# Kernel optimization log

Hardware: AMD Instinct MI355X
Metric: run time of the kernel (lower is better)

Reference implementation:

```python
import jax, jax.numpy as jnp
import numpy as np

HEADS = 3
NEG_SLOPE = 0.2


def setup_inputs() -> dict:
    key = jax.random.key(0)
    ks = jax.random.split(key, 16)
    B, node_num, his, in_dim = 2, 5000, 12, 2
    N = B * node_num
    E = 160000
    hidden = 32
    C = hidden * his  # 384, per-head out channels of GATConv
    gat_in = in_dim * his  # 24
    s = 0.05
    return {
        "x": jax.random.normal(ks[0], (B, node_num, his, in_dim), jnp.float32),
        "edge_index": jax.random.randint(ks[1], (2, E), 0, N, jnp.int64),
        "lin_w": jax.random.normal(ks[2], (HEADS * C, gat_in), jnp.float32) * s,
        "att_src": jax.random.normal(ks[3], (HEADS, C), jnp.float32) * s,
        "att_dst": jax.random.normal(ks[4], (HEADS, C), jnp.float32) * s,
        "gat_bias": jax.random.normal(ks[5], (C,), jnp.float32) * s,
        "w_ih": jax.random.normal(ks[6], (3 * hidden, hidden), jnp.float32) * s,
        "w_hh": jax.random.normal(ks[7], (3 * hidden, hidden), jnp.float32) * s,
        "b_ih": jax.random.normal(ks[8], (3 * hidden,), jnp.float32) * s,
        "b_hh": jax.random.normal(ks[9], (3 * hidden,), jnp.float32) * s,
        "p1_w": jax.random.normal(ks[10], (1, hidden), jnp.float32) * s,
        "p1_b": jax.random.normal(ks[11], (1,), jnp.float32) * s,
        "p2_w": jax.random.normal(ks[12], (his, his), jnp.float32) * s,
        "p2_b": jax.random.normal(ks[13], (his,), jnp.float32) * s,
    }


def _gat_conv(xf, src, dst, N, lin_w, att_src, att_dst, gat_bias):
    # xf: [N, gat_in]; returns [N, C] (mean over heads, concat=False)
    heads, C = att_src.shape
    h = (xf @ lin_w.T).reshape(N, heads, C)           # [N,heads,C]
    a_src = jnp.einsum('nhc,hc->nh', h, att_src)      # [N,heads]
    a_dst = jnp.einsum('nhc,hc->nh', h, att_dst)
    alpha = jax.nn.leaky_relu(a_src[src] + a_dst[dst], NEG_SLOPE)  # [E,heads]
    # edge softmax over incoming edges of each dst node (stable)
    amax = jax.ops.segment_max(alpha, dst, num_segments=N)
    ea = jnp.exp(alpha - amax[dst])
    denom = jax.ops.segment_sum(ea, dst, num_segments=N)
    w = ea / denom[dst]                               # [E,heads]
    msg = h[src] * w[:, :, None]                      # [E,heads,C] -- dominant traffic
    out = jax.ops.segment_sum(msg, dst, num_segments=N)
    return out.mean(axis=1) + gat_bias                # [N,C]


def _gru(seq, w_ih, w_hh, b_ih, b_hh):
    # seq: [N, T, H] -> outputs [N, T, H], PyTorch GRU gate order (r,z,n)
    N, T, H = seq.shape
    def step(hprev, xt):
        gi = xt @ w_ih.T + b_ih
        gh = hprev @ w_hh.T + b_hh
        ir, iz, inn = jnp.split(gi, 3, axis=-1)
        hr, hz, hn = jnp.split(gh, 3, axis=-1)
        r = jax.nn.sigmoid(ir + hr)
        z = jax.nn.sigmoid(iz + hz)
        n = jnp.tanh(inn + r * hn)
        hnew = (1.0 - z) * n + z * hprev
        return hnew, hnew
    h0 = jnp.zeros((N, H), seq.dtype)
    _, hs = jax.lax.scan(step, h0, seq.transpose(1, 0, 2))
    return hs.transpose(1, 0, 2)


def reference(x, edge_index, lin_w, att_src, att_dst, gat_bias,
              w_ih, w_hh, b_ih, b_hh, p1_w, p1_b, p2_w, p2_b):
    B, node_num, his, in_dim = x.shape
    N = B * node_num
    xf = x.reshape(N, his * in_dim)
    # GATConv adds self-loops (add_self_loops=True default in PyG)
    loops = jnp.arange(N)
    src = jnp.concatenate([edge_index[0], loops])
    dst = jnp.concatenate([edge_index[1], loops])
    gat_out = _gat_conv(xf, src, dst, N, lin_w, att_src, att_dst, gat_bias)  # [N, hidden*his]
    hidden = w_hh.shape[1]
    gru_in = gat_out.reshape(N, his, hidden)
    gru_out = _gru(gru_in, w_ih, w_hh, b_ih, b_hh)    # [N, his, hidden]
    o = (gru_out @ p1_w.T + p1_b).squeeze(-1)         # [N, his]
    o = o @ p2_w.T + p2_b                              # [N, pred_num]
    return o.reshape(B, node_num, -1)
```

## Files before the change

### kernel.cpp

```cpp
#include <hip/hip_runtime.h>
#include <math.h>

#define HEADS 3
#define C_OUT 384
#define GAT_IN 24
#define HID 32
#define TSTEPS 12
#define NEG_SLOPE 0.2f
#define CAPW 64
#define SLOTS 96

typedef __attribute__((ext_vector_type(8))) short bf16x8;
typedef __attribute__((ext_vector_type(4))) float f32x4;

__device__ __forceinline__ float sigm(float x) {
  return 1.f / (1.f + __expf(-x));
}
__device__ __forceinline__ float tanh_fast(float x) {
  return 2.f / (1.f + __expf(-2.f * x)) - 1.f;
}
__device__ __forceinline__ unsigned short f2bf(float x) {
  unsigned int u = __float_as_uint(x);
  unsigned int r = u + 0x7fffu + ((u >> 16) & 1u);
  return (unsigned short)(r >> 16);
}
__device__ __forceinline__ float bf2f(unsigned short u) {
  return __uint_as_float((unsigned int)u << 16);
}
__device__ __forceinline__ float lrelu(float x) {
  return x >= 0.f ? x : NEG_SLOPE * x;
}

__global__ __launch_bounds__(96) void k_const(const float* __restrict__ lin_w,
                                              const float* __restrict__ gat_bias,
                                              const float* __restrict__ wih,
                                              const float* __restrict__ bih,
                                              const float* __restrict__ att_src,
                                              const float* __restrict__ att_dst,
                                              unsigned short* __restrict__ WWt,
                                              float* __restrict__ biasb,
                                              float* __restrict__ vbuf,
                                              int* __restrict__ cnt, int N) {
  int b = blockIdx.x;
  if (b < 876) {
    int t = b / 73, k = b % 73;
    int g = threadIdx.x;
    __shared__ float s_w[32];
    if (g < 32) {
      if (k < 72) {
        int h = k / 24, j = k % 24;
        s_w[g] = lin_w[(size_t)(h * C_OUT + t * 32 + g) * GAT_IN + j] * (1.f / 3.f);
      } else {
        s_w[g] = gat_bias[t * 32 + g];
      }
    }
    __syncthreads();
    const float* wrow = wih + (size_t)g * 32;
    float acc = 0.f;
#pragma unroll
    for (int c = 0; c < 32; ++c) acc += s_w[c] * wrow[c];
    if (k < 72) {
      WWt[((size_t)t * 96 + g) * 96 + k] = f2bf(acc);
      if (k < 24) WWt[((size_t)t * 96 + g) * 96 + 72 + k] = 0;
    } else {
      biasb[t * 96 + g] = acc + bih[g];
    }
  } else if (b < 948) {
    int bb = b - 876;
    int h = bb / 24, j = bb % 24;
    int lane = threadIdx.x;
    if (lane >= 64) return;
    float as = 0.f, ad = 0.f;
    for (int c = lane; c < C_OUT; c += 64) {
      float wv = lin_w[(size_t)(h * C_OUT + c) * GAT_IN + j];
      as += att_src[h * C_OUT + c] * wv;
      ad += att_dst[h * C_OUT + c] * wv;
    }
#pragma unroll
    for (int off = 32; off >= 1; off >>= 1) {
      as += __shfl_xor(as, off, 64);
      ad += __shfl_xor(ad, off, 64);
    }
    if (lane == 0) {
      vbuf[h * 24 + j] = as;
      vbuf[72 + h * 24 + j] = ad;
    }
  } else {
    int i = (b - 948) * 96 + threadIdx.x;
    if (i < N) cnt[i] = 0;
  }
}

__global__ void k_place(const int* __restrict__ esrc,
                        const int* __restrict__ edst, int* __restrict__ cnt,
                        int* __restrict__ slist, int E, int ET) {
  int e = blockIdx.x * blockDim.x + threadIdx.x;
  if (e >= ET) return;
  int d, s;
  if (e < E) { d = edst[e]; s = esrc[e]; }
  else { d = e - E; s = e - E; }
  int pos = atomicAdd(&cnt[d], 1);
  if (pos < SLOTS) slist[(size_t)d * SLOTS + pos] = s;
}

__global__ __launch_bounds__(256) void k_aggx(
    const float* __restrict__ xf, const float* __restrict__ vbuf,
    const int* __restrict__ slist, const int* __restrict__ cnt,
    unsigned short* __restrict__ Yb, int N) {
  __shared__ float s_v[144];
  __shared__ float s_w[4][CAPW][3];
  __shared__ unsigned short s_xb[4][CAPW][26];
  int tid = threadIdx.x, lane = tid & 63, wv = tid >> 6;
  if (tid < 144) s_v[tid] = vbuf[tid];
  __syncthreads();
  int n = blockIdx.x * 4 + wv;
  if (n >= N) return;

  int deg = min(cnt[n], SLOTS);

  float xl = (lane < 24) ? xf[(size_t)n * 24 + lane] : 0.f;
  float ad0, ad1, ad2;
  {
    float p0 = (lane < 24) ? xl * s_v[72 + lane] : 0.f;
    float p1 = (lane < 24) ? xl * s_v[96 + lane] : 0.f;
    float p2 = (lane < 24) ? xl * s_v[120 + lane] : 0.f;
#pragma unroll
    for (int off = 32; off >= 1; off >>= 1) {
      p0 += __shfl_xor(p0, off, 64);
      p1 += __shfl_xor(p1, off, 64);
      p2 += __shfl_xor(p2, off, 64);
    }
    ad0 = p0; ad1 = p1; ad2 = p2;
  }

  float t0 = 0.f, t1 = 0.f, t2 = 0.f;
  for (int i = lane; i < deg; i += 64) {
    int s = slist[(size_t)n * SLOTS + i];
    const float4* xr = (const float4*)(xf + (size_t)s * 24);
    float xs[24];
#pragma unroll
    for (int q = 0; q < 6; ++q) {
      float4 v = xr[q];
      xs[4 * q] = v.x; xs[4 * q + 1] = v.y;
      xs[4 * q + 2] = v.z; xs[4 * q + 3] = v.w;
    }
    float as0 = 0.f, as1 = 0.f, as2 = 0.f;
#pragma unroll
    for (int j = 0; j < 24; ++j) {
      float v = xs[j];
      as0 += v * s_v[j];
      as1 += v * s_v[24 + j];
      as2 += v * s_v[48 + j];
    }
    float e0 = __expf(lrelu(as0 + ad0));
    float e1 = __expf(lrelu(as1 + ad1));
    float e2 = __expf(lrelu(as2 + ad2));
    if (i < CAPW) {
      s_w[wv][i][0] = e0; s_w[wv][i][1] = e1; s_w[wv][i][2] = e2;
#pragma unroll
      for (int j = 0; j < 24; ++j) s_xb[wv][i][j] = f2bf(xs[j]);
    }
    t0 += e0; t1 += e1; t2 += e2;
  }
#pragma unroll
  for (int off = 32; off >= 1; off >>= 1) {
    t0 += __shfl_xor(t0, off, 64);
    t1 += __shfl_xor(t1, off, 64);
    t2 += __shfl_xor(t2, off, 64);
  }
  float inv0 = 1.f / t0, inv1 = 1.f / t1, inv2 = 1.f / t2;

  int eg = lane >> 5;
  int c = lane & 31;
  float acc0 = 0.f, acc1 = 0.f, acc2 = 0.f;
  if (deg <= CAPW) {
    int cc = (c < 24) ? c : 0;
    float cmask = (c < 24) ? 1.f : 0.f;
#pragma unroll 2
    for (int i = eg; i < deg; i += 2) {
      float w0 = s_w[wv][i][0] * inv0;
      float w1 = s_w[wv][i][1] * inv1;
      float w2 = s_w[wv][i][2] * inv2;
      float xv = bf2f(s_xb[wv][i][cc]) * cmask;
      acc0 += w0 * xv; acc1 += w1 * xv; acc2 += w2 * xv;
    }
  } else {
    for (int i = eg; i < deg; i += 2) {
      int s = slist[(size_t)n * SLOTS + i];
      float as0 = 0.f, as1 = 0.f, as2 = 0.f;
      const float* xr = xf + (size_t)s * 24;
#pragma unroll
      for (int j = 0; j < 24; ++j) {
        float v = xr[j];
        as0 += v * s_v[j];
        as1 += v * s_v[24 + j];
        as2 += v * s_v[48 + j];
      }
      float w0 = __expf(lrelu(as0 + ad0)) * inv0;
      float w1 = __expf(lrelu(as1 + ad1)) * inv1;
      float w2 = __expf(lrelu(as2 + ad2)) * inv2;
      float xv = (c < 24) ? xf[(size_t)s * 24 + c] : 0.f;
      acc0 += w0 * xv; acc1 += w1 * xv; acc2 += w2 * xv;
    }
  }
  acc0 += __shfl_xor(acc0, 32, 64);
  acc1 += __shfl_xor(acc1, 32, 64);
  acc2 += __shfl_xor(acc2, 32, 64);
  if (lane < 24) {
    unsigned short* yr = Yb + (size_t)n * 72;
    yr[lane] = f2bf(acc0);
    yr[24 + lane] = f2bf(acc1);
    yr[48 + lane] = f2bf(acc2);
  }
}

__global__ __launch_bounds__(256, 2) void k_gmr(
    const unsigned short* __restrict__ Yb,
    const unsigned short* __restrict__ WWt, const float* __restrict__ biasb,
    const float* __restrict__ whh, const float* __restrict__ bhh,
    const float* __restrict__ p1w, const float* __restrict__ p1b,
    const float* __restrict__ p2w, const float* __restrict__ p2b,
    float* __restrict__ out, int N) {
  __shared__ short A_lds[16][104];
  __shared__ unsigned short gi_lds[12][16][96];
  __shared__ float s_bias[12][96];
  __shared__ float h_buf[4][36];
  __shared__ float s_o[16][12];
  int tid = threadIdx.x;
  int m0 = blockIdx.x * 16;

  const unsigned int* Yu = (const unsigned int*)Yb;
  for (int u = tid; u < 16 * 36; u += 256) {
    int r = u / 36, c2 = u % 36;
    int rc = min(m0 + r, N - 1);
    *(unsigned int*)&A_lds[r][c2 * 2] = Yu[(size_t)rc * 36 + c2];
  }
  if (tid < 256) {
    int r = tid >> 4, c2 = tid & 15;
    *(unsigned int*)&A_lds[r][72 + c2 * 2] = 0;
  }
  for (int u = tid; u < 12 * 96; u += 256) s_bias[u / 96][u % 96] = biasb[u];
  __syncthreads();

  int l = tid & 63, wv = tid >> 6;
  {
    int mrow = l & 15;
    int koff = (l >> 4) * 8;
    bf16x8 a0 = *(const bf16x8*)&A_lds[mrow][koff];
    bf16x8 a1 = *(const bf16x8*)&A_lds[mrow][32 + koff];
    bf16x8 a2 = *(const bf16x8*)&A_lds[mrow][64 + koff];
    int rrow = (l >> 4) * 4;
#pragma unroll
    for (int q = 0; q < 3; ++q) {
      int tt = wv * 3 + q;
#pragma unroll
      for (int nt = 0; nt < 6; ++nt) {
        int col = nt * 16 + (l & 15);
        const unsigned short* bp = WWt + ((size_t)tt * 96 + col) * 96 + koff;
        bf16x8 b0 = *(const bf16x8*)&bp[0];
        bf16x8 b1 = *(const bf16x8*)&bp[32];
        bf16x8 b2 = *(const bf16x8*)&bp[64];
        f32x4 acc = {0.f, 0.f, 0.f, 0.f};
        acc = __builtin_amdgcn_mfma_f32_16x16x32_bf16(a0, b0, acc, 0, 0, 0);
        acc = __builtin_amdgcn_mfma_f32_16x16x32_bf16(a1, b1, acc, 0, 0, 0);
        acc = __builtin_amdgcn_mfma_f32_16x16x32_bf16(a2, b2, acc, 0, 0, 0);
        float bs = s_bias[tt][col];
#pragma unroll
        for (int rg = 0; rg < 4; ++rg)
          gi_lds[tt][rrow + rg][col] = f2bf(acc[rg] + bs);
      }
    }
  }
  __syncthreads();

  int k = l & 31, jh = l >> 5;
  const float4* pr = (const float4*)(whh + (size_t)k * HID + jh * 16);
  const float4* pz = (const float4*)(whh + (size_t)(HID + k) * HID + jh * 16);
  const float4* pn = (const float4*)(whh + (size_t)(2 * HID + k) * HID + jh * 16);
  float4 wr0 = pr[0], wr1 = pr[1], wr2 = pr[2], wr3 = pr[3];
  float4 wz0 = pz[0], wz1 = pz[1], wz2 = pz[2], wz3 = pz[3];
  float4 wn0 = pn[0], wn1 = pn[1], wn2 = pn[2], wn3 = pn[3];
  float bhr = bhh[k], bhz = bhh[HID + k], bhn = bhh[2 * HID + k];
  float p1k = p1w[k];
  float p1b0 = p1b[0];

  for (int i = 0; i < 4; ++i) {
    int nl = wv * 4 + i;
    int node = m0 + nl;
    if (node >= N) break;
    if (jh == 0) h_buf[wv][k] = 0.f;
    float h = 0.f;
    float gr = bf2f(gi_lds[0][nl][k]);
    float gz = bf2f(gi_lds[0][nl][32 + k]);
    float gn = bf2f(gi_lds[0][nl][64 + k]);
    for (int t = 0; t < TSTEPS; ++t) {
      float gr1 = 0.f, gz1 = 0.f, gn1 = 0.f;
      if (t + 1 < TSTEPS) {
        gr1 = bf2f(gi_lds[t + 1][nl][k]);
        gz1 = bf2f(gi_lds[t + 1][nl][32 + k]);
        gn1 = bf2f(gi_lds[t + 1][nl][64 + k]);
      }
      const float* hh = &h_buf[wv][jh * 16];
      float4 h0 = *(const float4*)(hh);
      float4 h1 = *(const float4*)(hh + 4);
      float4 h2 = *(const float4*)(hh + 8);
      float4 h3 = *(const float4*)(hh + 12);
      float ar = wr0.x * h0.x + wr0.y * h0.y + wr0.z * h0.z + wr0.w * h0.w +
                 wr1.x * h1.x + wr1.y * h1.y + wr1.z * h1.z + wr1.w * h1.w +
                 wr2.x * h2.x + wr2.y * h2.y + wr2.z * h2.z + wr2.w * h2.w +
                 wr3.x * h3.x + wr3.y * h3.y + wr3.z * h3.z + wr3.w * h3.w;
      float az = wz0.x * h0.x + wz0.y * h0.y + wz0.z * h0.z + wz0.w * h0.w +
                 wz1.x * h1.x + wz1.y * h1.y + wz1.z * h1.z + wz1.w * h1.w +
                 wz2.x * h2.x + wz2.y * h2.y + wz2.z * h2.z + wz2.w * h2.w +
                 wz3.x * h3.x + wz3.y * h3.y + wz3.z * h3.z + wz3.w * h3.w;
      float an = wn0.x * h0.x + wn0.y * h0.y + wn0.z * h0.z + wn0.w * h0.w +
                 wn1.x * h1.x + wn1.y * h1.y + wn1.z * h1.z + wn1.w * h1.w +
                 wn2.x * h2.x + wn2.y * h2.y + wn2.z * h2.z + wn2.w * h2.w +
                 wn3.x * h3.x + wn3.y * h3.y + wn3.z * h3.z + wn3.w * h3.w;
      ar += __shfl_xor(ar, 32, 64);
      az += __shfl_xor(az, 32, 64);
      an += __shfl_xor(an, 32, 64);
      float r = sigm(gr + ar + bhr);
      float z = sigm(gz + az + bhz);
      float nn = tanh_fast(gn + r * (an + bhn));
      h = (1.f - z) * nn + z * h;
      if (jh == 0) h_buf[wv][k] = h;
      float po = p1k * h;
#pragma unroll
      for (int off = 16; off >= 1; off >>= 1) po += __shfl_xor(po, off, 64);
      if (l == 0) s_o[nl][t] = po + p1b0;
      gr = gr1; gz = gz1; gn = gn1;
    }
    if (l < TSTEPS) {
      float acc = p2b[l];
#pragma unroll
      for (int s2 = 0; s2 < TSTEPS; ++s2)
        acc += p2w[l * TSTEPS + s2] * s_o[nl][s2];
      out[(size_t)node * TSTEPS + l] = acc;
    }
  }
}

extern "C" void kernel_launch(void* const* d_in, const int* in_sizes, int n_in,
                              void* d_out, int out_size, void* d_ws,
                              size_t ws_size, hipStream_t stream) {
  const float* x = (const float*)d_in[0];
  const int* ei = (const int*)d_in[1];
  const float* lin_w = (const float*)d_in[2];
  const float* att_src = (const float*)d_in[3];
  const float* att_dst = (const float*)d_in[4];
  const float* gat_bias = (const float*)d_in[5];
  const float* w_ih = (const float*)d_in[6];
  const float* w_hh = (const float*)d_in[7];
  const float* b_ih = (const float*)d_in[8];
  const float* b_hh = (const float*)d_in[9];
  const float* p1w = (const float*)d_in[10];
  const float* p1b = (const float*)d_in[11];
  const float* p2w = (const float*)d_in[12];
  const float* p2b = (const float*)d_in[13];

  int N = in_sizes[0] / GAT_IN;
  int E = in_sizes[1] / 2;
  int ET = E + N;

  size_t off = 0;
  char* base = (char*)d_ws;
  auto alloc = [&](size_t bytes) {
    void* p = base + off;
    off += (bytes + 255) & ~(size_t)255;
    return p;
  };
  unsigned short* Yb = (unsigned short*)alloc((size_t)N * 72 * 2);
  unsigned short* WWt = (unsigned short*)alloc((size_t)12 * 96 * 96 * 2);
  float* biasb = (float*)alloc((size_t)12 * 96 * 4);
  float* vbuf = (float*)alloc(144 * 4);
  int* cnt = (int*)alloc((size_t)N * 4);
  int* slist = (int*)alloc((size_t)N * SLOTS * 4);
  (void)ws_size; (void)n_in; (void)out_size;

  int zero_blocks = (N + 95) / 96;
  k_const<<<948 + zero_blocks, 96, 0, stream>>>(lin_w, gat_bias, w_ih, b_ih,
                                                att_src, att_dst, WWt, biasb,
                                                vbuf, cnt, N);
  k_place<<<(ET + 255) / 256, 256, 0, stream>>>(ei, ei + E, cnt, slist, E, ET);
  k_aggx<<<(N + 3) / 4, 256, 0, stream>>>(x, vbuf, slist, cnt, Yb, N);
  k_gmr<<<(N + 15) / 16, 256, 0, stream>>>(Yb, WWt, biasb, w_hh, b_hh, p1w,
                                           p1b, p2w, p2b, (float*)d_out, N);
}
```

Baseline: 86.17 us.

## Run GRU recurrence on MFMA per 16-node wavefront, fusing input projection per step

Replaces the 256-thread GRU kernel with a single-wavefront kernel that handles 16 nodes at once. The hidden-state matmul (W_hh·h) now runs on bf16 MFMA across all 16 nodes, with h passed through a small LDS tile each step. The per-timestep input projection is computed inside the time loop instead of being staged into a large LDS buffer. This removes the scalar FMA dot products and the big shared-memory staging, at the cost of rounding W_hh and h to bf16 and adding a barrier every timestep.

```diff
diff --git a/kernel.cpp b/kernel.cpp
--- a/kernel.cpp
+++ b/kernel.cpp
@@ -214,129 +214,111 @@
   }
 }
 
-__global__ __launch_bounds__(256, 2) void k_gmr(
+__global__ __launch_bounds__(64) void k_rec2(
     const unsigned short* __restrict__ Yb,
     const unsigned short* __restrict__ WWt, const float* __restrict__ biasb,
     const float* __restrict__ whh, const float* __restrict__ bhh,
     const float* __restrict__ p1w, const float* __restrict__ p1b,
     const float* __restrict__ p2w, const float* __restrict__ p2b,
     float* __restrict__ out, int N) {
-  __shared__ short A_lds[16][104];
-  __shared__ unsigned short gi_lds[12][16][96];
-  __shared__ float s_bias[12][96];
-  __shared__ float h_buf[4][36];
+  __shared__ unsigned short h16[16][32];
   __shared__ float s_o[16][12];
-  int tid = threadIdx.x;
+  int l = threadIdx.x;
+  int c = l & 15, hi = l >> 4;
   int m0 = blockIdx.x * 16;
 
-  const unsigned int* Yu = (const unsigned int*)Yb;
-  for (int u = tid; u < 16 * 36; u += 256) {
-    int r = u / 36, c2 = u % 36;
-    int rc = min(m0 + r, N - 1);
-    *(unsigned int*)&A_lds[r][c2 * 2] = Yu[(size_t)rc * 36 + c2];
-  }
-  if (tid < 256) {
-    int r = tid >> 4, c2 = tid & 15;
-    *(unsigned int*)&A_lds[r][72 + c2 * 2] = 0;
-  }
-  for (int u = tid; u < 12 * 96; u += 256) s_bias[u / 96][u % 96] = biasb[u];
+  int row = min(m0 + c, N - 1);
+  const unsigned short* yr = Yb + (size_t)row * 72;
+  bf16x8 ya0 = *(const bf16x8*)(yr + hi * 8);
+  bf16x8 ya1 = *(const bf16x8*)(yr + 32 + hi * 8);
+  bf16x8 ya2 = {0, 0, 0, 0, 0, 0, 0, 0};
+  if (hi == 0) ya2 = *(const bf16x8*)(yr + 64);
+
+  bf16x8 wb[6];
+#pragma unroll
+  for (int nt = 0; nt < 6; ++nt) {
+    const float* wp = whh + (size_t)(nt * 16 + c) * 32 + hi * 8;
+#pragma unroll
+    for (int j = 0; j < 8; ++j) wb[nt][j] = (short)f2bf(wp[j]);
+  }
+
+  float bhr0 = bhh[c], bhr1 = bhh[c + 16];
+  float bhz0 = bhh[32 + c], bhz1 = bhh[48 + c];
+  float bhn0 = bhh[64 + c], bhn1 = bhh[80 + c];
+  float p1c0 = p1w[c], p1c1 = p1w[c + 16], p1b0 = p1b[0];
+
+  float hA[4] = {0.f, 0.f, 0.f, 0.f}, hB[4] = {0.f, 0.f, 0.f, 0.f};
+  bf16x8 ha = {0, 0, 0, 0, 0, 0, 0, 0};
+
+  for (int t = 0; t < TSTEPS; ++t) {
+    const unsigned short* Wt = WWt + (size_t)t * 96 * 96;
+    f32x4 g0 = {0,0,0,0}, g1 = {0,0,0,0}, g2 = {0,0,0,0};
+    f32x4 g3 = {0,0,0,0}, g4 = {0,0,0,0}, g5 = {0,0,0,0};
+#pragma unroll
+    for (int q = 0; q < 3; ++q) {
+      bf16x8 aq = (q == 0) ? ya0 : (q == 1) ? ya1 : ya2;
+      int ko = q * 32 + hi * 8;
+      bf16x8 b0 = *(const bf16x8*)(Wt + (size_t)(0 * 16 + c) * 96 + ko);
+      bf16x8 b1 = *(const bf16x8*)(Wt + (size_t)(1 * 16 + c) * 96 + ko);
+      bf16x8 b2 = *(const bf16x8*)(Wt + (size_t)(2 * 16 + c) * 96 + ko);
+      bf16x8 b3 = *(const bf16x8*)(Wt + (size_t)(3 * 16 + c) * 96 + ko);
+      bf16x8 b4 = *(const bf16x8*)(Wt + (size_t)(4 * 16 + c) * 96 + ko);
+      bf16x8 b5 = *(const bf16x8*)(Wt + (size_t)(5 * 16 + c) * 96 + ko);
+      g0 = __builtin_amdgcn_mfma_f32_16x16x32_bf16(aq, b0, g0, 0, 0, 0);
+      g1 = __builtin_amdgcn_mfma_f32_16x16x32_bf16(aq, b1, g1, 0, 0, 0);
+      g2 = __builtin_amdgcn_mfma_f32_16x16x32_bf16(aq, b2, g2, 0, 0, 0);
+      g3 = __builtin_amdgcn_mfma_f32_16x16x32_bf16(aq, b3, g3, 0, 0, 0);
+      g4 = __builtin_amdgcn_mfma_f32_16x16x32_bf16(aq, b4, g4, 0, 0, 0);
+      g5 = __builtin_amdgcn_mfma_f32_16x16x32_bf16(aq, b5, g5, 0, 0, 0);
+    }
+    f32x4 zz = {0,0,0,0};
+    f32x4 h0 = __builtin_amdgcn_mfma_f32_16x16x32_bf16(ha, wb[0], zz, 0, 0, 0);
+    f32x4 h1 = __builtin_amdgcn_mfma_f32_16x16x32_bf16(ha, wb[1], zz, 0, 0, 0);
+    f32x4 h2 = __builtin_amdgcn_mfma_f32_16x16x32_bf16(ha, wb[2], zz, 0, 0, 0);
+    f32x4 h3 = __builtin_amdgcn_mfma_f32_16x16x32_bf16(ha, wb[3], zz, 0, 0, 0);
+    f32x4 h4 = __builtin_amdgcn_mfma_f32_16x16x32_bf16(ha, wb[4], zz, 0, 0, 0);
+    f32x4 h5 = __builtin_amdgcn_mfma_f32_16x16x32_bf16(ha, wb[5], zz, 0, 0, 0);
+    const float* bt = biasb + t * 96;
+    float br0 = bt[c], br1 = bt[16 + c];
+    float bz0 = bt[32 + c], bz1 = bt[48 + c];
+    float bn0 = bt[64 + c], bn1 = bt[80 + c];
+    float po[4];
+#pragma unroll
+    for (int reg = 0; reg < 4; ++reg) {
+      float r0 = sigm(g0[reg] + br0 + h0[reg] + bhr0);
+      float z0 = sigm(g2[reg] + bz0 + h2[reg] + bhz0);
+      float n0 = tanh_fast(g4[reg] + bn0 + r0 * (h4[reg] + bhn0));
+      hA[reg] = (1.f - z0) * n0 + z0 * hA[reg];
+      float r1 = sigm(g1[reg] + br1 + h1[reg] + bhr1);
+      float z1 = sigm(g3[reg] + bz1 + h3[reg] + bhz1);
+      float n1 = tanh_fast(g5[reg] + bn1 + r1 * (h5[reg] + bhn1));
+      hB[reg] = (1.f - z1) * n1 + z1 * hB[reg];
+      h16[hi * 4 + reg][c] = f2bf(hA[reg]);
+      h16[hi * 4 + reg][c + 16] = f2bf(hB[reg]);
+      po[reg] = p1c0 * hA[reg] + p1c1 * hB[reg];
+    }
+#pragma unroll
+    for (int off = 1; off < 16; off <<= 1) {
+#pragma unroll
+      for (int reg = 0; reg < 4; ++reg) po[reg] += __shfl_xor(po[reg], off, 64);
+    }
+    if (c == 0) {
+#pragma unroll
+      for (int reg = 0; reg < 4; ++reg) s_o[hi * 4 + reg][t] = po[reg] + p1b0;
+    }
+    __syncthreads();
+    ha = *(const bf16x8*)&h16[c][hi * 8];
+  }
   __syncthreads();
-
-  int l = tid & 63, wv = tid >> 6;
-  {
-    int mrow = l & 15;
-    int koff = (l >> 4) * 8;
-    bf16x8 a0 = *(const bf16x8*)&A_lds[mrow][koff];
-    bf16x8 a1 = *(const bf16x8*)&A_lds[mrow][32 + koff];
-    bf16x8 a2 = *(const bf16x8*)&A_lds[mrow][64 + koff];
-    int rrow = (l >> 4) * 4;
-#pragma unroll
-    for (int q = 0; q < 3; ++q) {
-      int tt = wv * 3 + q;
-#pragma unroll
-      for (int nt = 0; nt < 6; ++nt) {
-        int col = nt * 16 + (l & 15);
-        const unsigned short* bp = WWt + ((size_t)tt * 96 + col) * 96 + koff;
-        bf16x8 b0 = *(const bf16x8*)&bp[0];
-        bf16x8 b1 = *(const bf16x8*)&bp[32];
-        bf16x8 b2 = *(const bf16x8*)&bp[64];
-        f32x4 acc = {0.f, 0.f, 0.f, 0.f};
-        acc = __builtin_amdgcn_mfma_f32_16x16x32_bf16(a0, b0, acc, 0, 0, 0);
-        acc = __builtin_amdgcn_mfma_f32_16x16x32_bf16(a1, b1, acc, 0, 0, 0);
-        acc = __builtin_amdgcn_mfma_f32_16x16x32_bf16(a2, b2, acc, 0, 0, 0);
-        float bs = s_bias[tt][col];
-#pragma unroll
-        for (int rg = 0; rg < 4; ++rg)
-          gi_lds[tt][rrow + rg][col] = f2bf(acc[rg] + bs);
-      }
-    }
-  }
-  __syncthreads();
-
-  int k = l & 31, jh = l >> 5;
-  const float4* pr = (const float4*)(whh + (size_t)k * HID + jh * 16);
-  const float4* pz = (const float4*)(whh + (size_t)(HID + k) * HID + jh * 16);
-  const float4* pn = (const float4*)(whh + (size_t)(2 * HID + k) * HID + jh * 16);
-  float4 wr0 = pr[0], wr1 = pr[1], wr2 = pr[2], wr3 = pr[3];
-  float4 wz0 = pz[0], wz1 = pz[1], wz2 = pz[2], wz3 = pz[3];
-  float4 wn0 = pn[0], wn1 = pn[1], wn2 = pn[2], wn3 = pn[3];
-  float bhr = bhh[k], bhz = bhh[HID + k], bhn = bhh[2 * HID + k];
-  float p1k = p1w[k];
-  float p1b0 = p1b[0];
-
-  for (int i = 0; i < 4; ++i) {
-    int nl = wv * 4 + i;
-    int node = m0 + nl;
-    if (node >= N) break;
-    if (jh == 0) h_buf[wv][k] = 0.f;
-    float h = 0.f;
-    float gr = bf2f(gi_lds[0][nl][k]);
-    float gz = bf2f(gi_lds[0][nl][32 + k]);
-    float gn = bf2f(gi_lds[0][nl][64 + k]);
-    for (int t = 0; t < TSTEPS; ++t) {
-      float gr1 = 0.f, gz1 = 0.f, gn1 = 0.f;
-      if (t + 1 < TSTEPS) {
-        gr1 = bf2f(gi_lds[t + 1][nl][k]);
-        gz1 = bf2f(gi_lds[t + 1][nl][32 + k]);
-        gn1 = bf2f(gi_lds[t + 1][nl][64 + k]);
-      }
-      const float* hh = &h_buf[wv][jh * 16];
-      float4 h0 = *(const float4*)(hh);
-      float4 h1 = *(const float4*)(hh + 4);
-      float4 h2 = *(const float4*)(hh + 8);
-      float4 h3 = *(const float4*)(hh + 12);
-      float ar = wr0.x * h0.x + wr0.y * h0.y + wr0.z * h0.z + wr0.w * h0.w +
-                 wr1.x * h1.x + wr1.y * h1.y + wr1.z * h1.z + wr1.w * h1.w +
-                 wr2.x * h2.x + wr2.y * h2.y + wr2.z * h2.z + wr2.w * h2.w +
-                 wr3.x * h3.x + wr3.y * h3.y + wr3.z * h3.z + wr3.w * h3.w;
-      float az = wz0.x * h0.x + wz0.y * h0.y + wz0.z * h0.z + wz0.w * h0.w +
-                 wz1.x * h1.x + wz1.y * h1.y + wz1.z * h1.z + wz1.w * h1.w +
-                 wz2.x * h2.x + wz2.y * h2.y + wz2.z * h2.z + wz2.w * h2.w +
-                 wz3.x * h3.x + wz3.y * h3.y + wz3.z * h3.z + wz3.w * h3.w;
-      float an = wn0.x * h0.x + wn0.y * h0.y + wn0.z * h0.z + wn0.w * h0.w +
-                 wn1.x * h1.x + wn1.y * h1.y + wn1.z * h1.z + wn1.w * h1.w +
-                 wn2.x * h2.x + wn2.y * h2.y + wn2.z * h2.z + wn2.w * h2.w +
-                 wn3.x * h3.x + wn3.y * h3.y + wn3.z * h3.z + wn3.w * h3.w;
-      ar += __shfl_xor(ar, 32, 64);
-      az += __shfl_xor(az, 32, 64);
-      an += __shfl_xor(an, 32, 64);
-      float r = sigm(gr + ar + bhr);
-      float z = sigm(gz + az + bhz);
-      float nn = tanh_fast(gn + r * (an + bhn));
-      h = (1.f - z) * nn + z * h;
-      if (jh == 0) h_buf[wv][k] = h;
-      float po = p1k * h;
-#pragma unroll
-      for (int off = 16; off >= 1; off >>= 1) po += __shfl_xor(po, off, 64);
-      if (l == 0) s_o[nl][t] = po + p1b0;
-      gr = gr1; gz = gz1; gn = gn1;
-    }
-    if (l < TSTEPS) {
-      float acc = p2b[l];
+  for (int idx = l; idx < 16 * TSTEPS; idx += 64) {
+    int node = idx / TSTEPS, tt = idx % TSTEPS;
+    int gn = m0 + node;
+    if (gn < N) {
+      float acc = p2b[tt];
 #pragma unroll
       for (int s2 = 0; s2 < TSTEPS; ++s2)
-        acc += p2w[l * TSTEPS + s2] * s_o[nl][s2];
-      out[(size_t)node * TSTEPS + l] = acc;
+        acc += p2w[tt * TSTEPS + s2] * s_o[node][s2];
+      out[(size_t)gn * TSTEPS + tt] = acc;
     }
   }
 }
@@ -384,6 +366,6 @@
                                                 vbuf, cnt, N);
   k_place<<<(ET + 255) / 256, 256, 0, stream>>>(ei, ei + E, cnt, slist, E, ET);
   k_aggx<<<(N + 3) / 4, 256, 0, stream>>>(x, vbuf, slist, cnt, Yb, N);
-  k_gmr<<<(N + 15) / 16, 256, 0, stream>>>(Yb, WWt, biasb, w_hh, b_hh, p1w,
+  k_rec2<<<(N + 15) / 16, 64, 0, stream>>>(Yb, WWt, biasb, w_hh, b_hh, p1w,
                                            p1b, p2w, p2b, (float*)d_out, N);
 }
```

Result: no change. 85.35 us (-0.9%).
